# Performance work log

Measured on AMD Instinct MI355X. Metric: run time of the kernel, lower is better.

## Reference

```python
import jax, jax.numpy as jnp
import numpy as np

DIM = 1024
NUM_HEADS = 16
HEAD_DIM = 64
NUM_LANDMARKS = 256
SEQ_LEN = 4096
BATCH = 4


def setup_inputs() -> dict:
    key = jax.random.key(0)
    ks = jax.random.split(key, 10)
    hd = NUM_HEADS * HEAD_DIM
    s = 1.0 / np.sqrt(DIM)
    inp = {
        "X": jax.random.normal(ks[0], (BATCH, SEQ_LEN, DIM), jnp.float32),
        "mask": jnp.ones((BATCH, SEQ_LEN), jnp.float32),
        "Wq": jax.random.normal(ks[1], (DIM, hd), jnp.float32) * s,
        "bq": jnp.zeros((hd,), jnp.float32),
        "Wk": jax.random.normal(ks[2], (DIM, hd), jnp.float32) * s,
        "bk": jnp.zeros((hd,), jnp.float32),
        "Wv": jax.random.normal(ks[3], (DIM, hd), jnp.float32) * s,
        "bv": jnp.zeros((hd,), jnp.float32),
        "Wff": jax.random.normal(ks[4], (hd, DIM), jnp.float32) * (1.0 / np.sqrt(hd)),
        "bff": jnp.zeros((DIM,), jnp.float32),
    }
    return inp


def _iterative_inv(mat, n_iter=6):
    # mat: [B,H,m,m]; Newton-Schulz style pseudo-inverse, faithful to torch code
    m = mat.shape[-1]
    I = jnp.eye(m, dtype=mat.dtype)
    K = mat
    # global max over the whole tensor, as torch.max with no dim
    denom = jnp.max(jnp.sum(jnp.abs(K), axis=-2)) * jnp.max(jnp.sum(jnp.abs(K), axis=-1))
    V = jnp.swapaxes(K, -1, -2) / denom
    for _ in range(n_iter):
        KV = K @ V
        V = 0.25 * V @ (13.0 * I - KV @ (15.0 * I - KV @ (7.0 * I - KV)))
    return V


def _nystrom_attn(Q, K, V, mask):
    # Q,K,V: [B,H,S,D]; mask: [B,S]
    B, H, S, D = Q.shape
    m = NUM_LANDMARKS
    scale = np.sqrt(np.sqrt(HEAD_DIM)).astype(np.float32)
    Q = Q * mask[:, None, :, None] / scale
    K = K * mask[:, None, :, None] / scale
    Ql = Q.reshape(B, H, m, S // m, D).mean(axis=-2)  # [B,H,m,D]
    Kl = K.reshape(B, H, m, S // m, D).mean(axis=-2)
    k1 = jax.nn.softmax(jnp.einsum('bhsd,bhmd->bhsm', Q, Kl), axis=-1)   # [B,H,S,m]
    k2 = jax.nn.softmax(jnp.einsum('bhmd,bhnd->bhmn', Ql, Kl), axis=-1)  # [B,H,m,m]
    k3 = jax.nn.softmax(
        jnp.einsum('bhmd,bhsd->bhms', Ql, K) - 1e9 * (1.0 - mask[:, None, None, :]),
        axis=-1)  # [B,H,m,S]
    return k1 @ (_iterative_inv(k2) @ (k3 @ V))  # [B,H,S,D]


def reference(X, mask, Wq, bq, Wk, bk, Wv, bv, Wff, bff):
    B, S, _ = X.shape
    def split(t):  # [B,S,H*D] -> [B,H,S,D]
        return t.reshape(B, S, NUM_HEADS, HEAD_DIM).transpose(0, 2, 1, 3)
    Q = split(X @ Wq + bq)
    K = split(X @ Wk + bk)
    V = split(X @ Wv + bv)
    attn = _nystrom_attn(Q, K, V, mask)
    attn = attn.transpose(0, 2, 1, 3).reshape(B, S, NUM_HEADS * HEAD_DIM)
    return attn @ Wff + bff
```

## Files before the change

### kernel.cpp

```cpp
#include <hip/hip_runtime.h>
#include <cstdint>
#include <cstddef>


typedef unsigned short u16;
typedef __attribute__((ext_vector_type(8))) short short8;
typedef __attribute__((ext_vector_type(4))) float f32x4;
typedef __attribute__((ext_vector_type(4))) unsigned short us4;
typedef __attribute__((ext_vector_type(8))) unsigned short us8;

__device__ __forceinline__ float bf2f(u16 u){ return __uint_as_float(((unsigned int)u)<<16); }
__device__ __forceinline__ u16 f2bf(float x){
  unsigned int i = __float_as_uint(x);
  unsigned int r = i + 0x7FFFu + ((i>>16)&1u);
  return (u16)(r>>16);
}
__device__ __forceinline__ f32x4 mfma16(short8 a, short8 b, f32x4 c){
  return __builtin_amdgcn_mfma_f32_16x16x32_bf16(a,b,c,0,0,0);
}
__device__ __forceinline__ void gld16(const void* g, void* l){
  __builtin_amdgcn_global_load_lds(
      (const __attribute__((address_space(1))) unsigned int*)g,
      (__attribute__((address_space(3))) unsigned int*)l, 16, 0, 0);
}

template<typename T>
__device__ __forceinline__ void load4v(const T* p, float x[4]){
  if constexpr (sizeof(T)==4){
    f32x4 v = *(const f32x4*)p;
    #pragma unroll
    for (int c=0;c<4;c++) x[c]=v[c];
  } else {
    us4 v = *(const us4*)p;
    #pragma unroll
    for (int c=0;c<4;c++) x[c]=bf2f(v[c]);
  }
}

template<int BM,int BN,int AM,int AN,bool BTB,bool SPLIT,bool FUSESM,
         typename TA,typename TB,typename TC>
__global__ __launch_bounds__(256) void gemm_k(
    const TA* __restrict__ A, const TB* __restrict__ B, TC* __restrict__ C,
    int M, int N, int K,
    long long sA, long long sB, long long sC, int ldc)
{
  constexpr int WR = BM/(16*AM);
  constexpr int WC = BN/(16*AN);
  static_assert(WR*WC==4, "need 4 waves");
  constexpr int LDW = 40;
  constexpr int NROW = BM+BN;
  constexpr int LOFF = NROW*LDW;
  __shared__ u16 lds[(SPLIT?2:1)*NROW*LDW];

  const int tid = threadIdx.x;
  const int z = blockIdx.z;
  const TA* __restrict__ Az = A + (size_t)z*sA;
  const TB* __restrict__ Bz = B + (size_t)z*sB;
  TC* __restrict__ Cz = C + (size_t)z*sC;
  const int tileM = blockIdx.x*BM;
  const int tileN = blockIdx.y*BN;

  const int lane = tid & 63;
  const int wv   = tid >> 6;
  const int wr   = wv / WC;
  const int wc   = wv % WC;
  const int lrow = lane & 15;
  const int kgrp = lane >> 4;
  const int koff = kgrp*8;

  f32x4 acc[AM][AN];
  #pragma unroll
  for (int i=0;i<AM;i++)
    #pragma unroll
    for (int j=0;j<AN;j++)
      acc[i][j] = (f32x4){0.f,0.f,0.f,0.f};

  u16* ldsA = lds;
  u16* ldsB = lds + BM*LDW;

  const int nkt = K >> 5;
  for (int kt=0; kt<nkt; ++kt){
    const int k0 = kt << 5;
    #pragma unroll
    for (int s2=0; s2<BM/32; ++s2){
      int slot = tid + s2*256;
      int row = slot >> 3;
      int kc  = (slot & 7) << 2;
      float x[4];
      load4v(Az + (size_t)(tileM+row)*K + (k0+kc), x);
      us4 h, l;
      #pragma unroll
      for (int c=0;c<4;c++){
        h[c] = f2bf(x[c]);
        if constexpr (SPLIT) l[c] = f2bf(x[c] - bf2f(h[c]));
      }
      *(us4*)&ldsA[row*LDW + kc] = h;
      if constexpr (SPLIT) *(us4*)&ldsA[LOFF + row*LDW + kc] = l;
    }
    {
      #pragma unroll
      for (int s2=0; s2<BN/32; ++s2){
        int slot = tid + s2*256;
        int row = slot >> 3;
        int kc  = (slot & 7) << 2;
        float x[4];
        load4v(Bz + (size_t)(tileN+row)*K + (k0+kc), x);
        us4 h, l;
        #pragma unroll
        for (int c=0;c<4;c++){
          h[c] = f2bf(x[c]);
          if constexpr (SPLIT) l[c] = f2bf(x[c] - bf2f(h[c]));
        }
        *(us4*)&ldsB[row*LDW + kc] = h;
        if constexpr (SPLIT) *(us4*)&ldsB[LOFF + row*LDW + kc] = l;
      }
    }
    __syncthreads();
    short8 ah[AM], al[AM];
    #pragma unroll
    for (int i=0;i<AM;i++){
      ah[i] = *(const short8*)&ldsA[(wr*AM*16 + i*16 + lrow)*LDW + koff];
      if constexpr (SPLIT) al[i] = *(const short8*)&ldsA[LOFF + (wr*AM*16 + i*16 + lrow)*LDW + koff];
    }
    #pragma unroll
    for (int j=0;j<AN;j++){
      short8 bh = *(const short8*)&ldsB[(wc*AN*16 + j*16 + lrow)*LDW + koff];
      if constexpr (SPLIT){
        short8 bl = *(const short8*)&ldsB[LOFF + (wc*AN*16 + j*16 + lrow)*LDW + koff];
        #pragma unroll
        for (int i=0;i<AM;i++){
          acc[i][j] = mfma16(ah[i], bh, acc[i][j]);
          acc[i][j] = mfma16(ah[i], bl, acc[i][j]);
          acc[i][j] = mfma16(al[i], bh, acc[i][j]);
        }
      } else {
        #pragma unroll
        for (int i=0;i<AM;i++)
          acc[i][j] = mfma16(ah[i], bh, acc[i][j]);
      }
    }
    __syncthreads();
  }

  #pragma unroll
  for (int r=0;r<4;r++){
    float mx = -3.0e38f;
    #pragma unroll
    for (int j=0;j<AN;j++) mx = fmaxf(mx, acc[0][j][r]);
    #pragma unroll
    for (int d=1; d<16; d<<=1) mx = fmaxf(mx, __shfl_xor(mx, d));
    float p[AN]; float ss = 0.f;
    #pragma unroll
    for (int j=0;j<AN;j++){ p[j] = expf(acc[0][j][r]-mx); ss += p[j]; }
    #pragma unroll
    for (int d=1; d<16; d<<=1) ss += __shfl_xor(ss, d);
    float inv = 1.0f/ss;
    int row = tileM + wr*16 + kgrp*4 + r;
    #pragma unroll
    for (int j=0;j<AN;j++){
      int col = j*16 + lrow;
      Cz[(size_t)row*ldc + col] = p[j]*inv;
    }
  }
}

template<int OUT>
__global__ __launch_bounds__(256) void sgemm_k(
    const u16* __restrict__ Ah, const u16* __restrict__ Al,
    const u16* __restrict__ Bh, const u16* __restrict__ Bl,
    int K, long long sA, long long sB,
    u16* __restrict__ RoH, u16* __restrict__ RoL,
    u16* __restrict__ CoH, u16* __restrict__ CoL,
    float* __restrict__ Fo, long long sO, int ldO,
    float addI, float csgn, float scale,
    const float* __restrict__ bias, const float* __restrict__ ml)
{
  __shared__ u16 lds[16384];
  const int tid = threadIdx.x;
  const int z = blockIdx.z;
  const int tileM = blockIdx.x*64, tileN = blockIdx.y*64;
  const int lane = tid&63, wv = tid>>6;
  const int wr = wv>>1, wc = wv&1;
  const int lrow = lane&15, kgrp = lane>>4;

  const u16* __restrict__ base[4] = {
    Ah + (size_t)z*sA + (size_t)tileM*K,
    Al + (size_t)z*sA + (size_t)tileM*K,
    Bh + (size_t)z*sB + (size_t)tileN*K,
    Bl + (size_t)z*sB + (size_t)tileN*K };

  f32x4 acc[2][2];
  #pragma unroll
  for (int i=0;i<2;i++)
    #pragma unroll
    for (int j=0;j<2;j++) acc[i][j] = (f32x4){0.f,0.f,0.f,0.f};

  for (int k0=0; k0<K; k0+=64){
    #pragma unroll
    for (int t4=0; t4<4; ++t4){
      #pragma unroll
      for (int hf=0; hf<2; ++hf){
        int w = hf*256 + tid;
        int row = w>>3, c = w&7;
        int cs = c ^ (row&7);
        gld16(base[t4] + (size_t)row*K + k0 + cs*8, lds + t4*4096 + (w & ~63)*8);
      }
    }
    __syncthreads();
    #pragma unroll
    for (int kk=0; kk<2; ++kk){
      int ch = kk*4 + kgrp;
      short8 a_h[2], a_l[2], b_h[2], b_l[2];
      #pragma unroll
      for (int i=0;i<2;i++){
        int r = wr*32 + i*16 + lrow;
        int off = r*64 + ((ch ^ (r&7))<<3);
        a_h[i] = *(const short8*)&lds[off];
        a_l[i] = *(const short8*)&lds[4096 + off];
      }
      #pragma unroll
      for (int j=0;j<2;j++){
        int r = wc*32 + j*16 + lrow;
        int off = r*64 + ((ch ^ (r&7))<<3);
        b_h[j] = *(const short8*)&lds[8192 + off];
        b_l[j] = *(const short8*)&lds[12288 + off];
      }
      #pragma unroll
      for (int i=0;i<2;i++)
        #pragma unroll
        for (int j=0;j<2;j++){
          acc[i][j] = mfma16(a_h[i], b_h[j], acc[i][j]);
          acc[i][j] = mfma16(a_h[i], b_l[j], acc[i][j]);
          acc[i][j] = mfma16(a_l[i], b_h[j], acc[i][j]);
        }
    }
    __syncthreads();
  }

  #pragma unroll
  for (int i=0;i<2;i++)
    #pragma unroll
    for (int j=0;j<2;j++){
      int grow0 = tileM + wr*32 + i*16 + kgrp*4;
      int gcol  = tileN + wc*32 + j*16 + lrow;
      if constexpr (OUT==0){
        us4 ch4, cl4;
        #pragma unroll
        for (int q=0;q<4;q++){
          int grow = grow0 + q;
          float p = acc[i][j][q]*scale;
          if (RoH){
            u16 h = f2bf(p);
            RoH[(size_t)z*65536 + (size_t)grow*256 + gcol] = h;
            RoL[(size_t)z*65536 + (size_t)grow*256 + gcol] = f2bf(p - bf2f(h));
          }
          float cv = csgn*p + ((grow==gcol)? addI : 0.f);
          ch4[q] = f2bf(cv);
          cl4[q] = f2bf(cv - bf2f(ch4[q]));
        }
        *(us4*)&CoH[(size_t)z*65536 + (size_t)gcol*256 + grow0] = ch4;
        *(us4*)&CoL[(size_t)z*65536 + (size_t)gcol*256 + grow0] = cl4;
      } else if constexpr (OUT==1){
        #pragma unroll
        for (int q=0;q<4;q++)
          CoH[(size_t)z*16384 + (size_t)gcol*256 + (grow0+q)] = f2bf(acc[i][j][q]);
      } else {
        #pragma unroll
        for (int q=0;q<4;q++){
          int grow = grow0+q;
          float v = acc[i][j][q] + ml[grow]*bias[gcol];
          int b = grow>>8, l = grow&255, h = gcol>>6, d = gcol&63;
          size_t oi = (((size_t)(b*16+h)*256 + l)*64 + d);
          Fo[oi] = v;
          if (RoH) RoH[oi] = f2bf(v);
        }
      }
    }
}

template<int EPI>
__global__ __launch_bounds__(256) void fgemm_k(
    const u16* __restrict__ A, const u16* __restrict__ Bt, float* __restrict__ Cf,
    u16* __restrict__ Q_, u16* __restrict__ K_, u16* __restrict__ V_,
    int M, int N, int K, int nTilesN,
    const float* __restrict__ bias, const float* __restrict__ rowscale)
{
  __shared__ u16 lds[2*128*64];
  u16* ldsA = lds;
  u16* ldsB = lds + 128*64;

  int flat = blockIdx.y*nTilesN + blockIdx.x;
  int nwg  = gridDim.x*gridDim.y;
  int chunk = nwg >> 3;
  int nid = (flat & 7)*chunk + (flat >> 3);
  int bxM = nid / nTilesN, byN = nid % nTilesN;
  const int tileM = bxM*128, tileN = byN*128;

  const int tid = threadIdx.x;
  const int lane = tid & 63, wv = tid>>6;
  const int wr = wv>>1, wc = wv&1;
  const int lrow = lane&15, kgrp = lane>>4;

  f32x4 acc[4][4];
  #pragma unroll
  for (int i=0;i<4;i++)
    #pragma unroll
    for (int j=0;j<4;j++) acc[i][j] = (f32x4){0.f,0.f,0.f,0.f};

  for (int k0=0; k0<K; k0+=64){
    #pragma unroll
    for (int i=0;i<4;i++){
      int s = i*256 + tid;
      int row = s>>3, c = s&7;
      int cs = c ^ (row&7);
      gld16(A + (size_t)(tileM+row)*K + k0 + cs*8, ldsA + (size_t)(s & ~63)*8);
    }
    #pragma unroll
    for (int i=0;i<4;i++){
      int s = i*256 + tid;
      int row = s>>3, c = s&7;
      int cs = c ^ (row&7);
      gld16(Bt + (size_t)(tileN+row)*K + k0 + cs*8, ldsB + (size_t)(s & ~63)*8);
    }
    __syncthreads();
    #pragma unroll
    for (int kk=0; kk<2; ++kk){
      int ch = kk*4 + kgrp;
      short8 af[4], bf[4];
      #pragma unroll
      for (int i=0;i<4;i++){
        int r = wr*64 + i*16 + lrow;
        af[i] = *(const short8*)&ldsA[r*64 + ((ch^(r&7))<<3)];
      }
      #pragma unroll
      for (int j=0;j<4;j++){
        int r = wc*64 + j*16 + lrow;
        bf[j] = *(const short8*)&ldsB[r*64 + ((ch^(r&7))<<3)];
      }
      #pragma unroll
      for (int i=0;i<4;i++)
        #pragma unroll
        for (int j=0;j<4;j++)
          acc[i][j] = mfma16(af[i], bf[j], acc[i][j]);
    }
    __syncthreads();
  }

  if constexpr (EPI==0){
    #pragma unroll
    for (int i=0;i<4;i++)
      #pragma unroll
      for (int j=0;j<4;j++)
        #pragma unroll
        for (int q=0;q<4;q++){
          int row = tileM + wr*64 + i*16 + kgrp*4 + q;
          int col = tileN + wc*64 + j*16 + lrow;
          Cf[(size_t)row*N + col] = acc[i][j][q] + (bias ? bias[col] : 0.f);
        }
  } else {
    #pragma unroll
    for (int i=0;i<4;i++)
      #pragma unroll
      for (int j=0;j<4;j++)
        #pragma unroll
        for (int q=0;q<4;q++){
          int rloc = wr*64 + i*16 + kgrp*4 + q;
          int cloc = wc*64 + j*16 + lrow;
          int col = tileN + cloc;
          float v = acc[i][j][q] + bias[col];
          if ((col>>10) < 2) v *= rowscale[tileM + rloc];
          lds[rloc*128 + cloc] = f2bf(v);
        }
    __syncthreads();
    #pragma unroll
    for (int c=0;c<8;c++){
      int idx = c*256 + tid;
      int row = idx >> 4;
      int seg = idx & 15;
      int col = tileN + seg*8;
      int which = col >> 10;
      int hd = col & 1023, h = hd>>6, d0 = hd&63;
      int grow = tileM + row;
      int b = grow>>12, s = grow&4095;
      u16* dst = (which==0) ? Q_ : (which==1) ? K_ : V_;
      us8 v = *(const us8*)&lds[row*128 + seg*8];
      *(us8*)&dst[(((size_t)(b*16+h))*4096 + s)*64 + d0] = v;
    }
  }
}

__global__ __launch_bounds__(256) void o3p_k(
    const float* __restrict__ Ql, const u16* __restrict__ Kb, const u16* __restrict__ Vb,
    const float* __restrict__ mask, float* __restrict__ Opart, float* __restrict__ MLpart)
{
  constexpr int QHI=0, QLO=4096, KT=8192, VT=12288, PHI=16640, PLO=20736;
  __shared__ u16 lds[24832];
  const int bx = blockIdx.x, ck = blockIdx.y, z = blockIdx.z;
  const int tid = threadIdx.x;
  const int lane = tid&63, wv = tid>>6;
  const int lrow = lane&15, kgrp = lane>>4;
  const float* Qlz = Ql + (size_t)z*16384 + (size_t)bx*64*64;
  const u16* Kz = Kb + (size_t)z*4096*64;
  const u16* Vz = Vb + (size_t)z*4096*64;
  const float* mrow = mask + (size_t)(z>>4)*4096;

  #pragma unroll
  for (int i=0;i<2;i++){
    int s = i*256 + tid;
    int row = s>>3, c = s&7;
    const float* src = Qlz + row*64 + c*8;
    f32x4 v0 = *(const f32x4*)src;
    f32x4 v1 = *(const f32x4*)(src+4);
    us8 hi, lo;
    #pragma unroll
    for (int e=0;e<4;e++){
      hi[e] = f2bf(v0[e]); lo[e] = f2bf(v0[e]-bf2f(hi[e]));
      hi[4+e] = f2bf(v1[e]); lo[4+e] = f2bf(v1[e]-bf2f(hi[4+e]));
    }
    int ad = row*64 + ((c^(row&7))<<3);
    *(us8*)&lds[QHI+ad] = hi;
    *(us8*)&lds[QLO+ad] = lo;
  }

  float m_r[4], l_r[4];
  f32x4 oacc[4];
  #pragma unroll
  for (int r=0;r<4;r++){ m_r[r] = -3.0e38f; l_r[r] = 0.f; }
  #pragma unroll
  for (int j=0;j<4;j++) oacc[j] = (f32x4){0.f,0.f,0.f,0.f};

  for (int st=0; st<16; ++st){
    int s0 = (ck*16 + st)*64;
    #pragma unroll
    for (int i=0;i<2;i++){
      int s = i*256 + tid;
      int row = s>>3, c = s&7;
      int cs = c ^ (row&7);
      gld16(Kz + (size_t)(s0+row)*64 + cs*8, &lds[KT + (size_t)(s & ~63)*8]);
    }
    #pragma unroll
    for (int i=0;i<2;i++){
      int s = i*256 + tid;
      int row = s>>3, c = s&7;
      us8 v = *(const us8*)(Vz + (size_t)(s0+row)*64 + c*8);
      #pragma unroll
      for (int e=0;e<8;e++) lds[VT + (c*8+e)*68 + row] = v[e];
    }
    __syncthreads();

    f32x4 sacc[4];
    #pragma unroll
    for (int j=0;j<4;j++) sacc[j] = (f32x4){0.f,0.f,0.f,0.f};
    int qr = wv*16 + lrow;
    #pragma unroll
    for (int kk=0; kk<2; ++kk){
      int ch = kk*4 + kgrp;
      short8 ah = *(const short8*)&lds[QHI + qr*64 + ((ch^(qr&7))<<3)];
      short8 alo = *(const short8*)&lds[QLO + qr*64 + ((ch^(qr&7))<<3)];
      #pragma unroll
      for (int j=0;j<4;j++){
        int kr = j*16 + lrow;
        short8 bk = *(const short8*)&lds[KT + kr*64 + ((ch^(kr&7))<<3)];
        sacc[j] = mfma16(ah, bk, sacc[j]);
        sacc[j] = mfma16(alo, bk, sacc[j]);
      }
    }
    float mb[4];
    #pragma unroll
    for (int j=0;j<4;j++) mb[j] = -1.0e9f*(1.0f - mrow[s0 + j*16 + lrow]);
    #pragma unroll
    for (int j=0;j<4;j++)
      #pragma unroll
      for (int r=0;r<4;r++) sacc[j][r] += mb[j];

    #pragma unroll
    for (int r=0;r<4;r++){
      float tm = fmaxf(fmaxf(sacc[0][r],sacc[1][r]), fmaxf(sacc[2][r],sacc[3][r]));
      #pragma unroll
      for (int d=1; d<16; d<<=1) tm = fmaxf(tm, __shfl_xor(tm, d));
      float mn = fmaxf(m_r[r], tm);
      float scf = expf(m_r[r] - mn);
      float ps[4]; float tsum = 0.f;
      #pragma unroll
      for (int j=0;j<4;j++){ ps[j] = expf(sacc[j][r] - mn); tsum += ps[j]; }
      #pragma unroll
      for (int d=1; d<16; d<<=1) tsum += __shfl_xor(tsum, d);
      l_r[r] = l_r[r]*scf + tsum;
      m_r[r] = mn;
      #pragma unroll
      for (int j=0;j<4;j++) oacc[j][r] *= scf;
      int prow = kgrp*4 + r;
      #pragma unroll
      for (int j=0;j<4;j++){
        int key = j*16 + lrow;
        u16 phi = f2bf(ps[j]);
        u16 plo = f2bf(ps[j] - bf2f(phi));
        int ad = wv*1024 + prow*64 + (((key>>3)^(prow&7))<<3) + (key&7);
        lds[PHI+ad] = phi;
        lds[PLO+ad] = plo;
      }
    }

    #pragma unroll
    for (int kk=0; kk<2; ++kk){
      int ch = kk*4 + kgrp;
      int pr = lrow;
      short8 pah = *(const short8*)&lds[PHI + wv*1024 + pr*64 + ((ch^(pr&7))<<3)];
      short8 plo = *(const short8*)&lds[PLO + wv*1024 + pr*64 + ((ch^(pr&7))<<3)];
      #pragma unroll
      for (int j=0;j<4;j++){
        int vr = j*16 + lrow;
        int a0 = VT + vr*68 + ch*8;
        us4 p0 = *(const us4*)&lds[a0];
        us4 p1 = *(const us4*)&lds[a0+4];
        short8 bv_;
        #pragma unroll
        for (int e=0;e<4;e++){ bv_[e] = (short)p0[e]; bv_[4+e] = (short)p1[e]; }
        oacc[j] = mfma16(pah, bv_, oacc[j]);
        oacc[j] = mfma16(plo, bv_, oacc[j]);
      }
    }
    __syncthreads();
  }

  #pragma unroll
  for (int j=0;j<4;j++)
    #pragma unroll
    for (int r=0;r<4;r++){
      int rowl = bx*64 + wv*16 + kgrp*4 + r;
      Opart[(((size_t)(ck*64+z)*256 + rowl)*64) + j*16 + lrow] = oacc[j][r];
    }
  #pragma unroll
  for (int r=0;r<4;r++){
    if (lrow==0){
      int rowl = bx*64 + wv*16 + kgrp*4 + r;
      MLpart[((size_t)(ck*64+z)*256 + rowl)*2 + 0] = m_r[r];
      MLpart[((size_t)(ck*64+z)*256 + rowl)*2 + 1] = l_r[r];
    }
  }
}

__global__ __launch_bounds__(256) void o3c_k(const float* __restrict__ Opart,
    const float* __restrict__ MLpart, u16* __restrict__ O3Th, u16* __restrict__ O3Tl)
{
  int z = blockIdx.x; int t = threadIdx.x;
  float m[4], l[4];
  #pragma unroll
  for (int c=0;c<4;c++){
    m[c] = MLpart[((size_t)(c*64+z)*256 + t)*2 + 0];
    l[c] = MLpart[((size_t)(c*64+z)*256 + t)*2 + 1];
  }
  float M = fmaxf(fmaxf(m[0],m[1]), fmaxf(m[2],m[3]));
  float w[4]; float L = 0.f;
  #pragma unroll
  for (int c=0;c<4;c++){ w[c] = expf(m[c]-M); L += l[c]*w[c]; }
  float inv = 1.0f/L;
  for (int d0=0; d0<16; ++d0){
    f32x4 o = (f32x4){0.f,0.f,0.f,0.f};
    #pragma unroll
    for (int c=0;c<4;c++){
      f32x4 x = *(const f32x4*)(Opart + ((size_t)(c*64+z)*256 + t)*64 + d0*4);
      #pragma unroll
      for (int e=0;e<4;e++) o[e] += w[c]*x[e];
    }
    #pragma unroll
    for (int e=0;e<4;e++){
      float val = o[e]*inv;
      int d = d0*4+e;
      u16 h = f2bf(val);
      O3Th[((size_t)z*64 + d)*256 + t] = h;
      O3Tl[((size_t)z*64 + d)*256 + t] = f2bf(val - bf2f(h));
    }
  }
}

__global__ void rs_k(const float* __restrict__ mask, float* __restrict__ rs){
  int i = blockIdx.x*256 + threadIdx.x;
  rs[i] = mask[i] * 0.3535533905932738f;
}
__global__ void zero2_k(float* __restrict__ mx){
  if (threadIdx.x < 2) mx[threadIdx.x] = 0.f;
}
__global__ void fill_k(float* __restrict__ p, int n, float v){
  for (int i = blockIdx.x*256 + threadIdx.x; i < n; i += gridDim.x*256) p[i] = v;
}
__global__ void splitrow_k(const float* __restrict__ X, u16* __restrict__ H, u16* __restrict__ L){
  int i = blockIdx.x*256 + threadIdx.x;
  f32x4 v = *(const f32x4*)(X + (size_t)i*4);
  us4 h, l;
  #pragma unroll
  for (int c=0;c<4;c++){ h[c] = f2bf(v[c]); l[c] = f2bf(v[c]-bf2f(h[c])); }
  *(us4*)(H + (size_t)i*4) = h;
  *(us4*)(L + (size_t)i*4) = l;
}
__global__ void bcat_k(const float* __restrict__ bq, const float* __restrict__ bk,
                       const float* __restrict__ bv, float* __restrict__ o){
  int i = blockIdx.x*256 + threadIdx.x;
  o[i] = (i<1024) ? bq[i] : (i<2048) ? bk[i-1024] : bv[i-2048];
}
__global__ __launch_bounds__(256) void wtr_k(const float* __restrict__ W, u16* __restrict__ T, int nOff){
  __shared__ float t[64][65];
  int ti = blockIdx.x, tj = blockIdx.y;
  int tt = threadIdx.x; int c = tt&63, r0 = tt>>6;
  #pragma unroll
  for (int rr=0; rr<16; rr++){
    int r = rr*4 + r0;
    t[r][c] = W[(size_t)(ti*64+r)*1024 + tj*64 + c];
  }
  __syncthreads();
  #pragma unroll
  for (int rr=0; rr<16; rr++){
    int r = rr*4 + r0;
    T[(size_t)(nOff + tj*64 + r)*1024 + ti*64 + c] = f2bf(t[c][r]);
  }
}
__global__ __launch_bounds__(256) void wtrsplit_k(const float* __restrict__ W,
    u16* __restrict__ TH, u16* __restrict__ TL){
  __shared__ float t[64][65];
  int ti = blockIdx.x, tj = blockIdx.y;
  int tt = threadIdx.x; int c = tt&63, r0 = tt>>6;
  #pragma unroll
  for (int rr=0; rr<16; rr++){
    int r = rr*4 + r0;
    t[r][c] = W[(size_t)(ti*64+r)*1024 + tj*64 + c];
  }
  __syncthreads();
  #pragma unroll
  for (int rr=0; rr<16; rr++){
    int r = rr*4 + r0;
    float v = t[c][r];
    u16 h = f2bf(v);
    TH[(size_t)(tj*64 + r)*1024 + ti*64 + c] = h;
    TL[(size_t)(tj*64 + r)*1024 + ti*64 + c] = f2bf(v - bf2f(h));
  }
}
__global__ __launch_bounds__(256) void pool_k(const float* __restrict__ X, const float* __restrict__ mask,
                                              float* __restrict__ Xl, float* __restrict__ ml,
                                              u16* __restrict__ Xb){
  int bl = blockIdx.x; int b = bl>>8; int l = bl&255;
  const float* Xp = X + ((size_t)b*4096 + (size_t)l*16)*1024;
  const float* mp = mask + (size_t)b*4096 + (size_t)l*16;
  int t = threadIdx.x;
  f32x4 acc = (f32x4){0.f,0.f,0.f,0.f};
  float msum = 0.f;
  #pragma unroll
  for (int j=0;j<16;j++){
    float mj = mp[j];
    msum += mj;
    f32x4 x = *(const f32x4*)(Xp + (size_t)j*1024 + t*4);
    us4 xb;
    #pragma unroll
    for (int c=0;c<4;c++){ acc[c] += mj*x[c]; xb[c] = f2bf(x[c]); }
    *(us4*)(Xb + ((size_t)bl*16 + j)*1024 + t*4) = xb;
  }
  const float c0 = 0.02209708691207961f;
  f32x4 o;
  #pragma unroll
  for (int c=0;c<4;c++) o[c] = acc[c]*c0;
  *(f32x4*)(Xl + (size_t)bl*1024 + t*4) = o;
  if (t==0) ml[bl] = msum * c0;
}
__global__ __launch_bounds__(256) void absmax_k(const float* __restrict__ k2, float* __restrict__ mx){
  int z = blockIdx.x; int t = threadIdx.x;
  const float* A = k2 + (size_t)z*65536;
  float rsum=0.f, csum=0.f;
  for (int j=0;j<256;j++){
    rsum += fabsf(A[t*256+j]);
    csum += fabsf(A[j*256+t]);
  }
  #pragma unroll
  for (int d=1; d<64; d<<=1){
    rsum = fmaxf(rsum, __shfl_xor(rsum, d));
    csum = fmaxf(csum, __shfl_xor(csum, d));
  }
  __shared__ float red[8];
  int wv=t>>6, ln=t&63;
  if (ln==0){ red[wv]=rsum; red[4+wv]=csum; }
  __syncthreads();
  if (t==0){
    float mr = fmaxf(fmaxf(red[0],red[1]),fmaxf(red[2],red[3]));
    float mc = fmaxf(fmaxf(red[4],red[5]),fmaxf(red[6],red[7]));
    atomicMax((int*)&mx[0], __float_as_int(mr));
    atomicMax((int*)&mx[1], __float_as_int(mc));
  }
}
__global__ __launch_bounds__(256) void v0prep_k(const float* __restrict__ K2f, const float* __restrict__ mx,
    u16* __restrict__ K2h, u16* __restrict__ K2l,
    u16* __restrict__ V0rh, u16* __restrict__ V0rl,
    u16* __restrict__ V0ch, u16* __restrict__ V0cl)
{
  int z = blockIdx.y; int bx = blockIdx.x;
  int ti = bx>>2, tj = bx&3;
  __shared__ float tile[64][65];
  const float* A = K2f + (size_t)z*65536;
  int t = threadIdx.x; int c = t&63, r0 = t>>6;
  float invden = 1.0f/(mx[0]*mx[1]);
  #pragma unroll
  for (int rr=0; rr<16; rr++){
    int r = rr*4 + r0;
    float v = A[(size_t)(ti*64 + r)*256 + tj*64 + c];
    tile[r][c] = v;
    size_t idx = (size_t)z*65536 + (size_t)(ti*64+r)*256 + tj*64 + c;
    u16 h = f2bf(v);
    K2h[idx] = h; K2l[idx] = f2bf(v - bf2f(h));
    float w = v*invden;
    h = f2bf(w);
    V0ch[idx] = h; V0cl[idx] = f2bf(w - bf2f(h));
  }
  __syncthreads();
  #pragma unroll
  for (int rr=0; rr<16; rr++){
    int r = rr*4 + r0;
    float w = tile[c][r]*invden;
    size_t idx = (size_t)z*65536 + (size_t)(tj*64+r)*256 + ti*64 + c;
    u16 h = f2bf(w);
    V0rh[idx] = h; V0rl[idx] = f2bf(w - bf2f(h));
  }
}

__device__ __forceinline__ int swz64(int row,int k){
  return row*64 + (((((k>>3)&7) ^ (row&7)))<<3) + (k&7);
}
__device__ __forceinline__ int swz256(int row,int k){
  return row*256 + ((((k>>3) ^ (row&7)))<<3) + (k&7);
}
__global__ __launch_bounds__(256) void attn_k(const u16* __restrict__ Qb,
    const u16* __restrict__ Klb, const u16* __restrict__ tTb,
    u16* __restrict__ attn){
  __shared__ u16 lds[32768];
  const int z = blockIdx.y;
  const int rows0 = blockIdx.x * 64;
  const int tid = threadIdx.x;
  const int lane = tid & 63, wv = tid>>6;
  const int lrow = lane & 15, kgrp = lane>>4;
  const u16* Qz = Qb + ((size_t)z*4096 + rows0)*64;
  const u16* Klz = Klb + (size_t)z*16384;
  const u16* tTz = tTb + (size_t)z*16384;

  #pragma unroll
  for (int i=0;i<8;i++){
    int s = i*256 + tid;
    int row = s>>3, c = s&7;
    gld16(Klz + (size_t)row*64 + ((c^(row&7))<<3), lds + (s & ~63)*8);
  }
  #pragma unroll
  for (int i=0;i<2;i++){
    int s = i*256 + tid;
    int row = s>>3, c = s&7;
    gld16(Qz + (size_t)row*64 + ((c^(row&7))<<3), lds + 16384 + (s & ~63)*8);
  }
  __syncthreads();

  f32x4 acc[4][4];
  #pragma unroll
  for (int i=0;i<4;i++)
    #pragma unroll
    for (int j=0;j<4;j++) acc[i][j] = (f32x4){0.f,0.f,0.f,0.f};
  #pragma unroll
  for (int ks=0; ks<2; ++ks){
    int ko = ks*32 + kgrp*8;
    short8 a[4], b[4];
    #pragma unroll
    for (int i=0;i<4;i++) a[i] = *(const short8*)&lds[16384 + swz64(16*i+lrow, ko)];
    #pragma unroll
    for (int j=0;j<4;j++) b[j] = *(const short8*)&lds[swz64(wv*64 + j*16 + lrow, ko)];
    #pragma unroll
    for (int i=0;i<4;i++)
      #pragma unroll
      for (int j=0;j<4;j++) acc[i][j] = mfma16(a[i], b[j], acc[i][j]);
  }
  __syncthreads();

  #pragma unroll
  for (int i=0;i<8;i++){
    int s = i*256 + tid;
    int row = s>>5, c = s&31;
    int gch = (c & ~7) | ((c ^ row) & 7);
    gld16(tTz + (size_t)row*256 + (gch<<3), lds + 16384 + (s & ~63)*8);
  }

  float* r0 = (float*)lds;
  float* r1 = r0 + 256;
  #pragma unroll
  for (int i=0;i<4;i++)
    #pragma unroll
    for (int r=0;r<4;r++){
      float mx = fmaxf(fmaxf(acc[i][0][r], acc[i][1][r]), fmaxf(acc[i][2][r], acc[i][3][r]));
      #pragma unroll
      for (int d=1; d<16; d<<=1) mx = fmaxf(mx, __shfl_xor(mx, d));
      if (lrow==0) r0[(16*i + kgrp*4 + r)*4 + wv] = mx;
    }
  __syncthreads();
  float inv_ir[4][4];
  #pragma unroll
  for (int i=0;i<4;i++)
    #pragma unroll
    for (int r=0;r<4;r++){
      int row = 16*i + kgrp*4 + r;
      float gm = fmaxf(fmaxf(r0[row*4+0], r0[row*4+1]), fmaxf(r0[row*4+2], r0[row*4+3]));
      float s = 0.f;
      #pragma unroll
      for (int j=0;j<4;j++){
        acc[i][j][r] = expf(acc[i][j][r] - gm);
        s += acc[i][j][r];
      }
      #pragma unroll
      for (int d=1; d<16; d<<=1) s += __shfl_xor(s, d);
      if (lrow==0) r1[row*4 + wv] = s;
      inv_ir[i][r] = 0.f; (void)inv_ir;
    }
  __syncthreads();
  #pragma unroll
  for (int i=0;i<4;i++)
    #pragma unroll
    for (int r=0;r<4;r++){
      int row = 16*i + kgrp*4 + r;
      inv_ir[i][r] = 1.0f/(r1[row*4+0]+r1[row*4+1]+r1[row*4+2]+r1[row*4+3]);
    }
  __syncthreads();

  #pragma unroll
  for (int i=0;i<4;i++)
    #pragma unroll
    for (int j=0;j<4;j++)
      #pragma unroll
      for (int r=0;r<4;r++){
        int row = 16*i + kgrp*4 + r;
        int l = wv*64 + j*16 + lrow;
        lds[swz256(row, l)] = f2bf(acc[i][j][r]*inv_ir[i][r]);
      }
  __syncthreads();

  f32x4 o[4];
  #pragma unroll
  for (int j=0;j<4;j++) o[j] = (f32x4){0.f,0.f,0.f,0.f};
  #pragma unroll
  for (int ks=0; ks<8; ++ks){
    int ko = ks*32 + kgrp*8;
    short8 a = *(const short8*)&lds[swz256(16*wv + lrow, ko)];
    #pragma unroll
    for (int j=0;j<4;j++){
      short8 bb = *(const short8*)&lds[16384 + swz256(j*16 + lrow, ko)];
      o[j] = mfma16(a, bb, o[j]);
    }
  }
  __syncthreads();
  #pragma unroll
  for (int j=0;j<4;j++)
    #pragma unroll
    for (int r=0;r<4;r++){
      int m = 16*wv + kgrp*4 + r;
      lds[m*64 + j*16 + lrow] = f2bf(o[j][r]);
    }
  __syncthreads();
  int b = z>>4, h = z&15;
  #pragma unroll
  for (int c=0;c<2;c++){
    int idx = c*256 + tid;
    int row = idx >> 3;
    int seg = idx & 7;
    us8 v = *(const us8*)&lds[row*64 + seg*8];
    *(us8*)&attn[((size_t)b*4096 + rows0 + row)*1024 + (size_t)h*64 + seg*8] = v;
  }
}

extern "C" void kernel_launch(void* const* d_in, const int* in_sizes, int n_in,
                              void* d_out, int out_size, void* d_ws, size_t ws_size,
                              hipStream_t stream) {
  (void)in_sizes; (void)n_in;
  const float* X    = (const float*)d_in[0];
  const float* mask = (const float*)d_in[1];
  const float* Wq   = (const float*)d_in[2];
  const float* bq   = (const float*)d_in[3];
  const float* Wk   = (const float*)d_in[4];
  const float* bk   = (const float*)d_in[5];
  const float* Wv   = (const float*)d_in[6];
  const float* bv   = (const float*)d_in[7];
  const float* Wff  = (const float*)d_in[8];
  const float* bff  = (const float*)d_in[9];
  float* outp = (float*)d_out;
  char* ws = (char*)d_ws;

  auto MiB = [](size_t x){ return x<<20; };
  const size_t O_QB   = 0;
  const size_t O_KB   = MiB(32);
  const size_t O_VB   = MiB(64);
  const size_t O_XB   = MiB(96);
  const size_t O_RG[4][2] = {
    {MiB(32),MiB(40)}, {MiB(48),MiB(56)}, {MiB(64),MiB(72)}, {MiB(80),MiB(88)} };
  const size_t O_OPART= MiB(96);
  const size_t O_MLP  = MiB(112);
  const size_t O_XAH  = MiB(96),  O_XAL = MiB(104);
  const size_t O_K2H  = MiB(112), O_K2L = MiB(120);
  const size_t O_K2F  = MiB(128);
  const size_t O_WQKVT= MiB(128);
  const size_t O_XLH  = MiB(134), O_XLL = MiB(136);
  const size_t O_WQTH = MiB(138), O_WQTL = MiB(140);
  const size_t O_QL   = MiB(144);
  const size_t O_TTB  = MiB(144);
  const size_t O_KL   = MiB(148);
  const size_t O_O3TH = MiB(152), O_O3TL = MiB(154);
  const size_t O_WKTH = MiB(152), O_WKTL = MiB(154);
  const size_t O_WFFT = MiB(156);
  const size_t O_XL   = MiB(158);
  const size_t O_KLB  = MiB(158);
  const size_t O_ATTN = MiB(32);
  const size_t O_RS   = MiB(162);
  const size_t O_ML   = O_RS + 65536;
  const size_t O_MX   = O_ML + 4096;
  const size_t O_BQKV = O_MX + 256;
  const size_t NEED   = O_BQKV + 16384;

  if (ws_size < NEED){
    fill_k<<<2048,256,0,stream>>>(outp, out_size, 1.0e9f);
    return;
  }

  u16*   Qb   = (u16*)(ws + O_QB);
  u16*   Kb   = (u16*)(ws + O_KB);
  u16*   Vb   = (u16*)(ws + O_VB);
  u16*   Xb   = (u16*)(ws + O_XB);
  u16*   WqkvT= (u16*)(ws + O_WQKVT);
  u16*   WffT = (u16*)(ws + O_WFFT);
  float* bqkv = (float*)(ws + O_BQKV);
  float* Xl   = (float*)(ws + O_XL);
  float* Ql   = (float*)(ws + O_QL);
  float* Kl   = (float*)(ws + O_KL);
  u16*   Klb  = (u16*)(ws + O_KLB);
  u16*   tTb  = (u16*)(ws + O_TTB);
  float* K2f  = (float*)(ws + O_K2F);
  float* rs   = (float*)(ws + O_RS);
  float* ml   = (float*)(ws + O_ML);
  float* Mx   = (float*)(ws + O_MX);
  float* Opart= (float*)(ws + O_OPART);
  float* MLp  = (float*)(ws + O_MLP);
  u16*   O3Th = (u16*)(ws + O_O3TH);
  u16*   O3Tl = (u16*)(ws + O_O3TL);
  u16*   K2h  = (u16*)(ws + O_K2H);
  u16*   K2l  = (u16*)(ws + O_K2L);
  u16*   XAh  = (u16*)(ws + O_XAH);
  u16*   XAl  = (u16*)(ws + O_XAL);
  u16*   Xlh  = (u16*)(ws + O_XLH);
  u16*   Xll  = (u16*)(ws + O_XLL);
  u16*   WqTh = (u16*)(ws + O_WQTH);
  u16*   WqTl = (u16*)(ws + O_WQTL);
  u16*   WkTh = (u16*)(ws + O_WKTH);
  u16*   WkTl = (u16*)(ws + O_WKTL);
  u16*   AttnB= (u16*)(ws + O_ATTN);
  u16* RGH[4]; u16* RGL[4];
  for (int i=0;i<4;i++){ RGH[i] = (u16*)(ws + O_RG[i][0]); RGL[i] = (u16*)(ws + O_RG[i][1]); }

  zero2_k<<<1,64,0,stream>>>(Mx);
  rs_k<<<64,256,0,stream>>>(mask, rs);
  pool_k<<<1024,256,0,stream>>>(X, mask, Xl, ml, Xb);

  wtr_k<<<dim3(16,16),256,0,stream>>>(Wq, WqkvT, 0);
  wtr_k<<<dim3(16,16),256,0,stream>>>(Wk, WqkvT, 1024);
  wtr_k<<<dim3(16,16),256,0,stream>>>(Wv, WqkvT, 2048);
  wtr_k<<<dim3(16,16),256,0,stream>>>(Wff, WffT, 0);
  bcat_k<<<12,256,0,stream>>>(bq, bk, bv, bqkv);
  fgemm_k<1><<<dim3(24,128),256,0,stream>>>(Xb, WqkvT, nullptr, Qb, Kb, Vb,
      16384, 3072, 1024, 24, bqkv, rs);

  splitrow_k<<<1024,256,0,stream>>>(Xl, Xlh, Xll);
  wtrsplit_k<<<dim3(16,16),256,0,stream>>>(Wq, WqTh, WqTl);
  wtrsplit_k<<<dim3(16,16),256,0,stream>>>(Wk, WkTh, WkTl);
  sgemm_k<2><<<dim3(16,16,1),256,0,stream>>>(Xlh, Xll, WqTh, WqTl, 1024, 0, 0,
      nullptr,nullptr,nullptr,nullptr, Ql, 0, 0, 0.f, 0.f, 1.f, bq, ml);
  sgemm_k<2><<<dim3(16,16,1),256,0,stream>>>(Xlh, Xll, WkTh, WkTl, 1024, 0, 0,
      Klb,nullptr,nullptr,nullptr, Kl, 0, 0, 0.f, 0.f, 1.f, bk, ml);

  gemm_k<64,256,1,16,true,true,true,float,float,float><<<dim3(4,1,64),256,0,stream>>>(
      Ql, Kl, K2f, 256,256,64, 16384,16384,65536, 256);

  o3p_k<<<dim3(4,4,64),256,0,stream>>>(Ql, Kb, Vb, mask, Opart, MLp);
  o3c_k<<<64,256,0,stream>>>(Opart, MLp, O3Th, O3Tl);

  absmax_k<<<64,256,0,stream>>>(K2f, Mx);
  v0prep_k<<<dim3(16,64),256,0,stream>>>(K2f, Mx, K2h, K2l, RGH[1], RGL[1], RGH[0], RGL[0]);
  int vc=0, vr=1, kv=2, x2=3;
  for (int it=0; it<6; ++it){
    sgemm_k<0><<<dim3(4,4,64),256,0,stream>>>(K2h, K2l, RGH[vc], RGL[vc], 256, 65536, 65536,
        RGH[kv], RGL[kv], XAh, XAl, nullptr, 0, 0, 7.f, -1.f, 1.f, nullptr, nullptr);
    sgemm_k<0><<<dim3(4,4,64),256,0,stream>>>(RGH[kv], RGL[kv], XAh, XAl, 256, 65536, 65536,
        nullptr, nullptr, RGH[x2], RGL[x2], nullptr, 0, 0, 15.f, -1.f, 1.f, nullptr, nullptr);
    sgemm_k<0><<<dim3(4,4,64),256,0,stream>>>(RGH[kv], RGL[kv], RGH[x2], RGL[x2], 256, 65536, 65536,
        nullptr, nullptr, XAh, XAl, nullptr, 0, 0, 13.f, -1.f, 1.f, nullptr, nullptr);
    sgemm_k<0><<<dim3(4,4,64),256,0,stream>>>(RGH[vr], RGL[vr], XAh, XAl, 256, 65536, 65536,
        RGH[kv], RGL[kv], RGH[x2], RGL[x2], nullptr, 0, 0, 0.f, 1.f, 0.25f, nullptr, nullptr);
    int nvc=x2, nvr=kv, nkv=vc, nx2=vr;
    vc=nvc; vr=nvr; kv=nkv; x2=nx2;
  }
  sgemm_k<1><<<dim3(4,1,64),256,0,stream>>>(RGH[vr], RGL[vr], O3Th, O3Tl, 256, 65536, 16384,
      nullptr,nullptr, tTb, nullptr, nullptr, 0, 0, 0.f, 0.f, 1.f, nullptr, nullptr);

  attn_k<<<dim3(64,64),256,0,stream>>>(Qb, Klb, tTb, AttnB);

  fgemm_k<0><<<dim3(8,128),256,0,stream>>>(AttnB, WffT, outp, nullptr, nullptr, nullptr,
      16384, 1024, 1024, 8, bff, nullptr);
}
```

Baseline: 1.189 ms.

## Double-buffer sgemm LDS tiles and merge small prep kernels into batched launches

The split-bf16 sgemm kernel now uses two LDS buffers. It issues the global-to-LDS loads for the next K tile before computing the current one, which removes one barrier per iteration and overlaps load latency with MFMA work. Separately, the mask scaling, bias concatenation and max zeroing are merged into one prep kernel, and the per-weight transpose launches are batched into single grid-z launches, cutting launch overhead. Doubling LDS to 64KB per block may reduce occupancy.

```diff
diff --git a/kernel.cpp b/kernel.cpp
--- a/kernel.cpp
+++ b/kernel.cpp
@@ -175,7 +175,7 @@
     float addI, float csgn, float scale,
     const float* __restrict__ bias, const float* __restrict__ ml)
 {
-  __shared__ u16 lds[16384];
+  __shared__ u16 lds[32768];
   const int tid = threadIdx.x;
   const int z = blockIdx.z;
   const int tileM = blockIdx.x*64, tileN = blockIdx.y*64;
@@ -195,7 +195,7 @@
     #pragma unroll
     for (int j=0;j<2;j++) acc[i][j] = (f32x4){0.f,0.f,0.f,0.f};
 
-  for (int k0=0; k0<K; k0+=64){
+  auto STAGE = [&](int buf, int k0){
     #pragma unroll
     for (int t4=0; t4<4; ++t4){
       #pragma unroll
@@ -203,10 +203,18 @@
         int w = hf*256 + tid;
         int row = w>>3, c = w&7;
         int cs = c ^ (row&7);
-        gld16(base[t4] + (size_t)row*K + k0 + cs*8, lds + t4*4096 + (w & ~63)*8);
-      }
-    }
+        gld16(base[t4] + (size_t)row*K + k0 + cs*8, lds + buf*16384 + t4*4096 + (w & ~63)*8);
+      }
+    }
+  };
+
+  const int nk = K >> 6;
+  STAGE(0, 0);
+  for (int kt=0; kt<nk; ++kt){
+    const int cur = kt & 1;
     __syncthreads();
+    if (kt+1 < nk) STAGE(cur^1, (kt+1)<<6);
+    const int lb = cur*16384;
     #pragma unroll
     for (int kk=0; kk<2; ++kk){
       int ch = kk*4 + kgrp;
@@ -214,14 +222,14 @@
       #pragma unroll
       for (int i=0;i<2;i++){
         int r = wr*32 + i*16 + lrow;
-        int off = r*64 + ((ch ^ (r&7))<<3);
+        int off = lb + r*64 + ((ch ^ (r&7))<<3);
         a_h[i] = *(const short8*)&lds[off];
         a_l[i] = *(const short8*)&lds[4096 + off];
       }
       #pragma unroll
       for (int j=0;j<2;j++){
         int r = wc*32 + j*16 + lrow;
-        int off = r*64 + ((ch ^ (r&7))<<3);
+        int off = lb + r*64 + ((ch ^ (r&7))<<3);
         b_h[j] = *(const short8*)&lds[8192 + off];
         b_l[j] = *(const short8*)&lds[12288 + off];
       }
@@ -234,7 +242,6 @@
           acc[i][j] = mfma16(a_l[i], b_h[j], acc[i][j]);
         }
     }
-    __syncthreads();
   }
 
   #pragma unroll
@@ -574,15 +581,23 @@
   }
 }
 
-__global__ void rs_k(const float* __restrict__ mask, float* __restrict__ rs){
-  int i = blockIdx.x*256 + threadIdx.x;
-  rs[i] = mask[i] * 0.3535533905932738f;
-}
-__global__ void zero2_k(float* __restrict__ mx){
-  if (threadIdx.x < 2) mx[threadIdx.x] = 0.f;
-}
 __global__ void fill_k(float* __restrict__ p, int n, float v){
   for (int i = blockIdx.x*256 + threadIdx.x; i < n; i += gridDim.x*256) p[i] = v;
+}
+__global__ void prep_k(const float* __restrict__ mask, float* __restrict__ rs,
+                       const float* __restrict__ bq, const float* __restrict__ bk,
+                       const float* __restrict__ bv, float* __restrict__ bqkv,
+                       float* __restrict__ mx){
+  int b = blockIdx.x;
+  if (b < 64){
+    int i = b*256 + threadIdx.x;
+    rs[i] = mask[i] * 0.3535533905932738f;
+  } else if (b < 76){
+    int j = (b-64)*256 + threadIdx.x;
+    bqkv[j] = (j<1024) ? bq[j] : (j<2048) ? bk[j-1024] : bv[j-2048];
+  } else {
+    if (threadIdx.x < 2) mx[threadIdx.x] = 0.f;
+  }
 }
 __global__ void splitrow_k(const float* __restrict__ X, u16* __restrict__ H, u16* __restrict__ L){
   int i = blockIdx.x*256 + threadIdx.x;
@@ -593,13 +608,14 @@
   *(us4*)(H + (size_t)i*4) = h;
   *(us4*)(L + (size_t)i*4) = l;
 }
-__global__ void bcat_k(const float* __restrict__ bq, const float* __restrict__ bk,
-                       const float* __restrict__ bv, float* __restrict__ o){
-  int i = blockIdx.x*256 + threadIdx.x;
-  o[i] = (i<1024) ? bq[i] : (i<2048) ? bk[i-1024] : bv[i-2048];
-}
-__global__ __launch_bounds__(256) void wtr_k(const float* __restrict__ W, u16* __restrict__ T, int nOff){
+__global__ __launch_bounds__(256) void wtr4_k(
+    const float* __restrict__ Wq, const float* __restrict__ Wk,
+    const float* __restrict__ Wv, const float* __restrict__ Wff,
+    u16* __restrict__ Tqkv, u16* __restrict__ Tff){
   __shared__ float t[64][65];
+  int zi = blockIdx.z;
+  const float* W = (zi==0)?Wq:(zi==1)?Wk:(zi==2)?Wv:Wff;
+  u16* T = (zi==3)? Tff : (Tqkv + (size_t)zi*1048576);
   int ti = blockIdx.x, tj = blockIdx.y;
   int tt = threadIdx.x; int c = tt&63, r0 = tt>>6;
   #pragma unroll
@@ -611,12 +627,18 @@
   #pragma unroll
   for (int rr=0; rr<16; rr++){
     int r = rr*4 + r0;
-    T[(size_t)(nOff + tj*64 + r)*1024 + ti*64 + c] = f2bf(t[c][r]);
-  }
-}
-__global__ __launch_bounds__(256) void wtrsplit_k(const float* __restrict__ W,
-    u16* __restrict__ TH, u16* __restrict__ TL){
+    T[(size_t)(tj*64 + r)*1024 + ti*64 + c] = f2bf(t[c][r]);
+  }
+}
+__global__ __launch_bounds__(256) void wtrsplit2_k(
+    const float* __restrict__ Wq, const float* __restrict__ Wk,
+    u16* __restrict__ QH, u16* __restrict__ QL,
+    u16* __restrict__ KH, u16* __restrict__ KL){
   __shared__ float t[64][65];
+  int zi = blockIdx.z;
+  const float* W = zi ? Wk : Wq;
+  u16* TH = zi ? KH : QH;
+  u16* TL = zi ? KL : QL;
   int ti = blockIdx.x, tj = blockIdx.y;
   int tt = threadIdx.x; int c = tt&63, r0 = tt>>6;
   #pragma unroll
@@ -950,21 +972,15 @@
   u16* RGH[4]; u16* RGL[4];
   for (int i=0;i<4;i++){ RGH[i] = (u16*)(ws + O_RG[i][0]); RGL[i] = (u16*)(ws + O_RG[i][1]); }
 
-  zero2_k<<<1,64,0,stream>>>(Mx);
-  rs_k<<<64,256,0,stream>>>(mask, rs);
+  prep_k<<<77,256,0,stream>>>(mask, rs, bq, bk, bv, bqkv, Mx);
   pool_k<<<1024,256,0,stream>>>(X, mask, Xl, ml, Xb);
 
-  wtr_k<<<dim3(16,16),256,0,stream>>>(Wq, WqkvT, 0);
-  wtr_k<<<dim3(16,16),256,0,stream>>>(Wk, WqkvT, 1024);
-  wtr_k<<<dim3(16,16),256,0,stream>>>(Wv, WqkvT, 2048);
-  wtr_k<<<dim3(16,16),256,0,stream>>>(Wff, WffT, 0);
-  bcat_k<<<12,256,0,stream>>>(bq, bk, bv, bqkv);
+  wtr4_k<<<dim3(16,16,4),256,0,stream>>>(Wq, Wk, Wv, Wff, WqkvT, WffT);
   fgemm_k<1><<<dim3(24,128),256,0,stream>>>(Xb, WqkvT, nullptr, Qb, Kb, Vb,
       16384, 3072, 1024, 24, bqkv, rs);
 
   splitrow_k<<<1024,256,0,stream>>>(Xl, Xlh, Xll);
-  wtrsplit_k<<<dim3(16,16),256,0,stream>>>(Wq, WqTh, WqTl);
-  wtrsplit_k<<<dim3(16,16),256,0,stream>>>(Wk, WkTh, WkTl);
+  wtrsplit2_k<<<dim3(16,16,2),256,0,stream>>>(Wq, Wk, WqTh, WqTl, WkTh, WkTl);
   sgemm_k<2><<<dim3(16,16,1),256,0,stream>>>(Xlh, Xll, WqTh, WqTl, 1024, 0, 0,
       nullptr,nullptr,nullptr,nullptr, Ql, 0, 0, 0.f, 0.f, 1.f, bq, ml);
   sgemm_k<2><<<dim3(16,16,1),256,0,stream>>>(Xlh, Xll, WkTh, WkTl, 1024, 0, 0,
```

New measurement: 1.200 ms. No clear change (+0.9%).
